# Performance work log

Measured on AMD Instinct MI355X. Metric: run time of the kernel, lower is better.

The kernel has to match this reference:

```python
import jax, jax.numpy as jnp
import numpy as np

L, D, H, FF = 24, 512, 16, 2048   # n_layer, hidden_dim, heads, mlp hidden
XLEN, YLEN = 1024, 1024
EPS = 1e-5


def setup_inputs() -> dict:
    key = jax.random.key(0)
    ks = jax.random.split(key, 6)
    S = XLEN + YLEN
    s = 0.02
    return {
        "x": jax.random.normal(ks[0], (1, S, D), jnp.float32),
        "qkv_w": jax.random.normal(ks[1], (L, 3 * D, D), jnp.float32) * s,
        "qkv_b": jnp.zeros((L, 3 * D), jnp.float32),
        "out_w": jax.random.normal(ks[2], (L, D, D), jnp.float32) * s,
        "out_b": jnp.zeros((L, D), jnp.float32),
        "w1": jax.random.normal(ks[3], (L, FF, D), jnp.float32) * s,
        "b1": jnp.zeros((L, FF), jnp.float32),
        "w2": jax.random.normal(ks[4], (L, D, FF), jnp.float32) * s,
        "b2": jnp.zeros((L, D), jnp.float32),
        "norm_w1": jnp.ones((L, D), jnp.float32),
        "norm_b1": jnp.zeros((L, D), jnp.float32),
        "norm_w2": jnp.ones((L, D), jnp.float32),
        "norm_b2": jnp.zeros((L, D), jnp.float32),
        "x_len": XLEN,
        "y_len": YLEN,
    }


def _layer_norm(h, w, b):
    m = h.mean(-1, keepdims=True)
    v = ((h - m) ** 2).mean(-1, keepdims=True)
    return (h - m) * jax.lax.rsqrt(v + EPS) * w + b


def _build_mask(x_len, y_len):
    # text rows: attend to all text, never to audio; audio rows: causal over audio, full over text
    top = jnp.concatenate([jnp.zeros((x_len, x_len), bool), jnp.ones((x_len, y_len), bool)], axis=1)
    bot = jnp.concatenate([jnp.zeros((y_len, x_len), bool), jnp.triu(jnp.ones((y_len, y_len), bool), 1)], axis=1)
    bm = jnp.concatenate([top, bot], axis=0)
    # canonical_mask: bool -> additive float with -100000 at masked positions
    return jnp.where(bm, jnp.float32(-100000.0), jnp.float32(0.0))


def reference(x, qkv_w, qkv_b, out_w, out_b, w1, b1, w2, b2, norm_w1, norm_b1, norm_w2, norm_b2, x_len, y_len):
    B, S, _ = x.shape
    hd = D // H
    scale = 1.0 / np.sqrt(hd)
    mask = _build_mask(x_len, y_len)  # [S, S]

    def layer(h, p):
        qw, qb, ow, ob, W1, B1, W2, B2, nw1, nb1, nw2, nb2 = p
        qkv = h @ qw.T + qb                                   # [B,S,3D]
        q, k, v = jnp.split(qkv, 3, axis=-1)
        q = q.reshape(B, S, H, hd).transpose(0, 2, 1, 3)      # [B,H,S,hd]
        k = k.reshape(B, S, H, hd).transpose(0, 2, 1, 3)
        v = v.reshape(B, S, H, hd).transpose(0, 2, 1, 3)
        att = jax.nn.softmax(jnp.einsum('bhqd,bhkd->bhqk', q, k) * scale + mask, axis=-1)
        o = jnp.einsum('bhqk,bhkd->bhqd', att, v).transpose(0, 2, 1, 3).reshape(B, S, D)
        o = o @ ow.T + ob
        h = _layer_norm(h + o, nw1, nb1)
        m = jax.nn.relu(h @ W1.T + B1) @ W2.T + B2            # T2SMLP
        h = _layer_norm(h + m, nw2, nb2)
        return h, None

    params = (qkv_w, qkv_b, out_w, out_b, w1, b1, w2, b2, norm_w1, norm_b1, norm_w2, norm_b2)
    x, _ = jax.lax.scan(layer, x, params)
    return x
```

## Files before the change

### kernel.cpp

```cpp
#include <hip/hip_runtime.h>
#include <cstddef>

#define S_LEN 2048
#define XLEN_C 1024
#define DMODEL 512
#define NHEAD 16
#define HDIM 32
#define FFDIM 2048
#define NLAYER 24
#define TD3 1536

typedef __attribute__((ext_vector_type(4))) float f32x4;
typedef __attribute__((ext_vector_type(8))) short short8;

__device__ __forceinline__ void split2(float x, unsigned short& h, unsigned short& l) {
  unsigned u = __float_as_uint(x);
  unsigned r = u + 0x7FFFu + ((u >> 16) & 1u);
  h = (unsigned short)(r >> 16);
  float hf = __uint_as_float((unsigned)h << 16);
  float lo = x - hf;
  unsigned u2 = __float_as_uint(lo);
  unsigned r2 = u2 + 0x7FFFu + ((u2 >> 16) & 1u);
  l = (unsigned short)(r2 >> 16);
}

template<int WMF, bool RELU, bool SPLIT_OUT>
__global__ __launch_bounds__(256) void gemm_mfma(const unsigned short* __restrict__ Ahg,
                                                 const unsigned short* __restrict__ Alg,
                                                 const float* __restrict__ Bg,
                                                 const float* __restrict__ bias,
                                                 float* __restrict__ Cf,
                                                 unsigned short* __restrict__ Ch,
                                                 unsigned short* __restrict__ Cl,
                                                 int N, int K) {
  constexpr int BM = 32 * WMF;
  __shared__ __align__(16) unsigned short Ahs[BM][40];
  __shared__ __align__(16) unsigned short Als[BM][40];
  __shared__ __align__(16) unsigned short Bhs[64][40];
  __shared__ __align__(16) unsigned short Bls[64][40];

  const int tid  = threadIdx.x;
  const int m0   = blockIdx.y * BM;
  const int n0   = blockIdx.x << 6;
  const int w    = tid >> 6;
  const int lane = tid & 63;
  const int wm   = (w >> 1) * (16 * WMF);
  const int wn   = (w & 1) << 5;
  const int fr   = lane & 15;
  const int fq   = lane >> 4;

  const int br = tid >> 2, bc = (tid & 3) << 3;

  f32x4 acc[WMF][2];
  #pragma unroll
  for (int i = 0; i < WMF; ++i)
    #pragma unroll
    for (int j = 0; j < 2; ++j)
      acc[i][j] = (f32x4){0.f, 0.f, 0.f, 0.f};

  for (int k0 = 0; k0 < K; k0 += 32) {
    float4 b0 = *(const float4*)&Bg[(size_t)(n0 + br) * K + k0 + bc];
    float4 b1 = *(const float4*)&Bg[(size_t)(n0 + br) * K + k0 + bc + 4];
    short8 bh, bl;
    {
      const float bf[8] = {b0.x, b0.y, b0.z, b0.w, b1.x, b1.y, b1.z, b1.w};
      #pragma unroll
      for (int i = 0; i < 8; ++i) {
        unsigned short h, lo; split2(bf[i], h, lo);
        bh[i] = (short)h; bl[i] = (short)lo;
      }
    }
    short8 a_h[(BM * 4) / 256], a_l[(BM * 4) / 256];
    #pragma unroll
    for (int it = 0; it < (BM * 4) / 256; ++it) {
      const int c = tid + (it << 8);
      const int arow = c >> 2, acol = (c & 3) << 3;
      a_h[it] = *(const short8*)&Ahg[(size_t)(m0 + arow) * K + k0 + acol];
      a_l[it] = *(const short8*)&Alg[(size_t)(m0 + arow) * K + k0 + acol];
    }
    __syncthreads();
    #pragma unroll
    for (int it = 0; it < (BM * 4) / 256; ++it) {
      const int c = tid + (it << 8);
      const int arow = c >> 2, acol = (c & 3) << 3;
      *(short8*)&Ahs[arow][acol] = a_h[it];
      *(short8*)&Als[arow][acol] = a_l[it];
    }
    *(short8*)&Bhs[br][bc] = bh;
    *(short8*)&Bls[br][bc] = bl;
    __syncthreads();

    short8 fah[WMF], fal[WMF], fbh[2], fbl[2];
    #pragma unroll
    for (int fm = 0; fm < WMF; ++fm) {
      fah[fm] = *(const short8*)&Ahs[wm + (fm << 4) + fr][fq << 3];
      fal[fm] = *(const short8*)&Als[wm + (fm << 4) + fr][fq << 3];
    }
    #pragma unroll
    for (int fn = 0; fn < 2; ++fn) {
      fbh[fn] = *(const short8*)&Bhs[wn + (fn << 4) + fr][fq << 3];
      fbl[fn] = *(const short8*)&Bls[wn + (fn << 4) + fr][fq << 3];
    }
    #pragma unroll
    for (int fm = 0; fm < WMF; ++fm)
      #pragma unroll
      for (int fn = 0; fn < 2; ++fn) {
        acc[fm][fn] = __builtin_amdgcn_mfma_f32_16x16x32_bf16(fah[fm], fbh[fn], acc[fm][fn], 0, 0, 0);
        acc[fm][fn] = __builtin_amdgcn_mfma_f32_16x16x32_bf16(fah[fm], fbl[fn], acc[fm][fn], 0, 0, 0);
        acc[fm][fn] = __builtin_amdgcn_mfma_f32_16x16x32_bf16(fal[fm], fbh[fn], acc[fm][fn], 0, 0, 0);
      }
  }

  #pragma unroll
  for (int fn = 0; fn < 2; ++fn) {
    const int col = n0 + wn + (fn << 4) + fr;
    const float bb = bias[col];
    #pragma unroll
    for (int fm = 0; fm < WMF; ++fm) {
      const int rbase = m0 + wm + (fm << 4) + (fq << 2);
      #pragma unroll
      for (int i = 0; i < 4; ++i) {
        float v = acc[fm][fn][i] + bb;
        if (RELU) v = fmaxf(v, 0.f);
        const size_t idx = (size_t)(rbase + i) * N + col;
        if (SPLIT_OUT) {
          unsigned short h, lo; split2(v, h, lo);
          Ch[idx] = h; Cl[idx] = lo;
        } else {
          Cf[idx] = v;
        }
      }
    }
  }
}

__global__ __launch_bounds__(256) void attn_mfma(const unsigned short* __restrict__ qh_g,
                                                 const unsigned short* __restrict__ ql_g,
                                                 unsigned short* __restrict__ oh_g,
                                                 unsigned short* __restrict__ ol_g) {
  const int hh  = blockIdx.x;
  const int q0  = blockIdx.y << 6;
  const int tid = threadIdx.x;
  const int w   = tid >> 6;
  const int lane = tid & 63;
  const int fr = lane & 15;
  const int fq = lane >> 4;
  constexpr float SCALE = 0.17677669529663687f;

  __shared__ __align__(16) unsigned short Kh[64][40];
  __shared__ __align__(16) unsigned short Kl[64][40];
  __shared__ __align__(16) unsigned short Vth[32][72];
  __shared__ __align__(16) unsigned short Vtl[32][72];
  __shared__ __align__(16) unsigned short Ph[4][16][72];
  __shared__ __align__(16) unsigned short Pl[4][16][72];

  const int qrow = q0 + (w << 4) + fr;
  const short8 fQh = *(const short8*)&qh_g[(size_t)qrow * TD3 + hh * HDIM + (fq << 3)];
  const short8 fQl = *(const short8*)&ql_g[(size_t)qrow * TD3 + hh * HDIM + (fq << 3)];

  float m = -3.0e38f, l = 0.f;
  f32x4 accO[2];
  accO[0] = (f32x4){0.f, 0.f, 0.f, 0.f};
  accO[1] = (f32x4){0.f, 0.f, 0.f, 0.f};

  const int kend   = (q0 < XLEN_C) ? XLEN_C : (q0 + 64);
  const int ntiles = kend >> 6;

  const int krow = tid >> 2, kcol = (tid & 3) << 3;
  const int vd = tid & 31, vseg = tid >> 5;

  for (int t = 0; t < ntiles; ++t) {
    const int c0 = t << 6;
    __syncthreads();
    *(short8*)&Kh[krow][kcol] =
        *(const short8*)&qh_g[(size_t)(c0 + krow) * TD3 + DMODEL + hh * HDIM + kcol];
    *(short8*)&Kl[krow][kcol] =
        *(const short8*)&ql_g[(size_t)(c0 + krow) * TD3 + DMODEL + hh * HDIM + kcol];
    short8 vh8, vl8;
    #pragma unroll
    for (int j = 0; j < 8; ++j) {
      const size_t ga = (size_t)(c0 + (vseg << 3) + j) * TD3 + 2 * DMODEL + hh * HDIM + vd;
      vh8[j] = (short)qh_g[ga];
      vl8[j] = (short)ql_g[ga];
    }
    *(short8*)&Vth[vd][vseg << 3] = vh8;
    *(short8*)&Vtl[vd][vseg << 3] = vl8;
    __syncthreads();

    f32x4 s4[4];
    #pragma unroll
    for (int sub = 0; sub < 4; ++sub) {
      s4[sub] = (f32x4){0.f, 0.f, 0.f, 0.f};
      const short8 kh = *(const short8*)&Kh[(sub << 4) + fr][fq << 3];
      const short8 kl = *(const short8*)&Kl[(sub << 4) + fr][fq << 3];
      s4[sub] = __builtin_amdgcn_mfma_f32_16x16x32_bf16(kh, fQh, s4[sub], 0, 0, 0);
      s4[sub] = __builtin_amdgcn_mfma_f32_16x16x32_bf16(kh, fQl, s4[sub], 0, 0, 0);
      s4[sub] = __builtin_amdgcn_mfma_f32_16x16x32_bf16(kl, fQh, s4[sub], 0, 0, 0);
    }

    float sv[16];
    float tmax = -3.0e38f;
    #pragma unroll
    for (int sub = 0; sub < 4; ++sub)
      #pragma unroll
      for (int i = 0; i < 4; ++i) {
        const int k = c0 + (sub << 4) + (fq << 2) + i;
        const bool ok = (k < XLEN_C) | (k <= qrow);
        const float val = ok ? s4[sub][i] * SCALE : -3.0e38f;
        sv[(sub << 2) + i] = val;
        tmax = fmaxf(tmax, val);
      }
    tmax = fmaxf(tmax, __shfl_xor(tmax, 16));
    tmax = fmaxf(tmax, __shfl_xor(tmax, 32));
    const float mnew  = fmaxf(m, tmax);
    const float alpha = __expf(m - mnew);
    m = mnew;
    float psum = 0.f;
    unsigned short p_h[16], p_l[16];
    #pragma unroll
    for (int idx = 0; idx < 16; ++idx) {
      const float p = __expf(sv[idx] - mnew);
      psum += p;
      split2(p, p_h[idx], p_l[idx]);
    }
    psum += __shfl_xor(psum, 16);
    psum += __shfl_xor(psum, 32);
    l = l * alpha + psum;

    #pragma unroll
    for (int sub = 0; sub < 4; ++sub) {
      ushort4 uh, ul;
      uh.x = p_h[(sub << 2) + 0]; uh.y = p_h[(sub << 2) + 1];
      uh.z = p_h[(sub << 2) + 2]; uh.w = p_h[(sub << 2) + 3];
      ul.x = p_l[(sub << 2) + 0]; ul.y = p_l[(sub << 2) + 1];
      ul.z = p_l[(sub << 2) + 2]; ul.w = p_l[(sub << 2) + 3];
      *(ushort4*)&Ph[w][fr][(sub << 4) + (fq << 2)] = uh;
      *(ushort4*)&Pl[w][fr][(sub << 4) + (fq << 2)] = ul;
    }

    const float a0 = __shfl(alpha, (fq << 2) + 0);
    const float a1 = __shfl(alpha, (fq << 2) + 1);
    const float a2 = __shfl(alpha, (fq << 2) + 2);
    const float a3 = __shfl(alpha, (fq << 2) + 3);
    #pragma unroll
    for (int df = 0; df < 2; ++df) {
      accO[df][0] *= a0; accO[df][1] *= a1;
      accO[df][2] *= a2; accO[df][3] *= a3;
    }

    #pragma unroll
    for (int kh2 = 0; kh2 < 2; ++kh2) {
      const short8 pah = *(const short8*)&Ph[w][fr][(kh2 << 5) + (fq << 3)];
      const short8 pal = *(const short8*)&Pl[w][fr][(kh2 << 5) + (fq << 3)];
      #pragma unroll
      for (int df = 0; df < 2; ++df) {
        const short8 vbh = *(const short8*)&Vth[(df << 4) + fr][(kh2 << 5) + (fq << 3)];
        const short8 vbl = *(const short8*)&Vtl[(df << 4) + fr][(kh2 << 5) + (fq << 3)];
        accO[df] = __builtin_amdgcn_mfma_f32_16x16x32_bf16(pah, vbh, accO[df], 0, 0, 0);
        accO[df] = __builtin_amdgcn_mfma_f32_16x16x32_bf16(pal, vbh, accO[df], 0, 0, 0);
        accO[df] = __builtin_amdgcn_mfma_f32_16x16x32_bf16(pah, vbl, accO[df], 0, 0, 0);
      }
    }
  }

  const float linv = 1.f / l;
  const float l0 = __shfl(linv, (fq << 2) + 0);
  const float l1 = __shfl(linv, (fq << 2) + 1);
  const float l2v = __shfl(linv, (fq << 2) + 2);
  const float l3 = __shfl(linv, (fq << 2) + 3);
  #pragma unroll
  for (int df = 0; df < 2; ++df) {
    const int col = hh * HDIM + (df << 4) + fr;
    const float vals[4] = {accO[df][0] * l0, accO[df][1] * l1,
                           accO[df][2] * l2v, accO[df][3] * l3};
    #pragma unroll
    for (int i = 0; i < 4; ++i) {
      const int row = q0 + (w << 4) + (fq << 2) + i;
      unsigned short h, lo; split2(vals[i], h, lo);
      oh_g[(size_t)row * DMODEL + col] = h;
      ol_g[(size_t)row * DMODEL + col] = lo;
    }
  }
}

__global__ __launch_bounds__(256) void add_layernorm(const float* __restrict__ h,
                                                     const float* __restrict__ r,
                                                     const float* __restrict__ w,
                                                     const float* __restrict__ b,
                                                     float* __restrict__ out,
                                                     unsigned short* __restrict__ oh,
                                                     unsigned short* __restrict__ ol) {
  const int row = blockIdx.x;
  const int tid = threadIdx.x;
  const float2 hv = *(const float2*)&h[(size_t)row * DMODEL + tid * 2];
  const float2 rv = *(const float2*)&r[(size_t)row * DMODEL + tid * 2];
  const float a0 = hv.x + rv.x, a1 = hv.y + rv.y;
  float s = a0 + a1, ss = a0 * a0 + a1 * a1;
  #pragma unroll
  for (int off = 32; off; off >>= 1) {
    s  += __shfl_xor(s, off);
    ss += __shfl_xor(ss, off);
  }
  __shared__ float sb[4], ssb[4];
  const int wid = tid >> 6;
  if ((tid & 63) == 0) { sb[wid] = s; ssb[wid] = ss; }
  __syncthreads();
  s  = sb[0] + sb[1] + sb[2] + sb[3];
  ss = ssb[0] + ssb[1] + ssb[2] + ssb[3];
  const float mean = s * (1.f / DMODEL);
  const float var  = ss * (1.f / DMODEL) - mean * mean;
  const float rs   = rsqrtf(var + 1e-5f);
  const float2 wv = *(const float2*)&w[tid * 2];
  const float2 bv = *(const float2*)&b[tid * 2];
  const float o0 = (a0 - mean) * rs * wv.x + bv.x;
  const float o1 = (a1 - mean) * rs * wv.y + bv.y;
  float2 o; o.x = o0; o.y = o1;
  *(float2*)&out[(size_t)row * DMODEL + tid * 2] = o;
  unsigned short h0, l0, h1, l1;
  split2(o0, h0, l0); split2(o1, h1, l1);
  ushort2 uh; uh.x = h0; uh.y = h1;
  ushort2 ul; ul.x = l0; ul.y = l1;
  *(ushort2*)&oh[(size_t)row * DMODEL + tid * 2] = uh;
  *(ushort2*)&ol[(size_t)row * DMODEL + tid * 2] = ul;
}

__global__ __launch_bounds__(256) void split_init(const float* __restrict__ x,
                                                  float* __restrict__ f,
                                                  unsigned short* __restrict__ h,
                                                  unsigned short* __restrict__ l,
                                                  int n4) {
  const int i = blockIdx.x * 256 + threadIdx.x;
  if (i >= n4) return;
  const float4 v = *(const float4*)&x[i * 4];
  *(float4*)&f[i * 4] = v;
  const float vf[4] = {v.x, v.y, v.z, v.w};
  ushort4 uh, ul;
  unsigned short hh, ll;
  split2(vf[0], hh, ll); uh.x = hh; ul.x = ll;
  split2(vf[1], hh, ll); uh.y = hh; ul.y = ll;
  split2(vf[2], hh, ll); uh.z = hh; ul.z = ll;
  split2(vf[3], hh, ll); uh.w = hh; ul.w = ll;
  *(ushort4*)&h[i * 4] = uh;
  *(ushort4*)&l[i * 4] = ul;
}

extern "C" void kernel_launch(void* const* d_in, const int* in_sizes, int n_in,
                              void* d_out, int out_size, void* d_ws, size_t ws_size,
                              hipStream_t stream) {
  const float* x     = (const float*)d_in[0];
  const float* qkv_w = (const float*)d_in[1];
  const float* qkv_b = (const float*)d_in[2];
  const float* out_w = (const float*)d_in[3];
  const float* out_b = (const float*)d_in[4];
  const float* w1    = (const float*)d_in[5];
  const float* b1    = (const float*)d_in[6];
  const float* w2    = (const float*)d_in[7];
  const float* b2    = (const float*)d_in[8];
  const float* nw1   = (const float*)d_in[9];
  const float* nb1   = (const float*)d_in[10];
  const float* nw2   = (const float*)d_in[11];
  const float* nb2   = (const float*)d_in[12];

  char* p = (char*)d_ws;
  float* Hc = (float*)p;              p += (size_t)S_LEN * DMODEL * 4;
  unsigned short* Hh = (unsigned short*)p;   p += (size_t)S_LEN * DMODEL * 2;
  unsigned short* Hl = (unsigned short*)p;   p += (size_t)S_LEN * DMODEL * 2;
  unsigned short* qkvh = (unsigned short*)p; p += (size_t)S_LEN * TD3 * 2;
  unsigned short* qkvl = (unsigned short*)p; p += (size_t)S_LEN * TD3 * 2;
  unsigned short* oath = (unsigned short*)p; p += (size_t)S_LEN * DMODEL * 2;
  unsigned short* oatl = (unsigned short*)p; p += (size_t)S_LEN * DMODEL * 2;
  float* opr = (float*)p;             p += (size_t)S_LEN * DMODEL * 4;
  unsigned short* midh = (unsigned short*)p; p += (size_t)S_LEN * FFDIM * 2;
  unsigned short* midl = (unsigned short*)p; p += (size_t)S_LEN * FFDIM * 2;

  split_init<<<(S_LEN * DMODEL / 4 + 255) / 256, 256, 0, stream>>>(
      x, Hc, Hh, Hl, S_LEN * DMODEL / 4);

  for (int l = 0; l < NLAYER; ++l) {
    const float* qw = qkv_w + (size_t)l * TD3 * DMODEL;
    const float* qb = qkv_b + (size_t)l * TD3;
    const float* ow = out_w + (size_t)l * DMODEL * DMODEL;
    const float* ob = out_b + (size_t)l * DMODEL;
    const float* W1 = w1 + (size_t)l * FFDIM * DMODEL;
    const float* B1 = b1 + (size_t)l * FFDIM;
    const float* W2 = w2 + (size_t)l * DMODEL * FFDIM;
    const float* B2 = b2 + (size_t)l * DMODEL;

    gemm_mfma<4, false, true><<<dim3(TD3 / 64, S_LEN / 128), 256, 0, stream>>>(
        Hh, Hl, qw, qb, nullptr, qkvh, qkvl, TD3, DMODEL);
    attn_mfma<<<dim3(NHEAD, S_LEN / 64), 256, 0, stream>>>(qkvh, qkvl, oath, oatl);
    gemm_mfma<2, false, false><<<dim3(DMODEL / 64, S_LEN / 64), 256, 0, stream>>>(
        oath, oatl, ow, ob, opr, nullptr, nullptr, DMODEL, DMODEL);
    add_layernorm<<<S_LEN, 256, 0, stream>>>(
        Hc, opr, nw1 + (size_t)l * DMODEL, nb1 + (size_t)l * DMODEL, Hc, Hh, Hl);
    gemm_mfma<4, true, true><<<dim3(FFDIM / 64, S_LEN / 128), 256, 0, stream>>>(
        Hh, Hl, W1, B1, nullptr, midh, midl, FFDIM, DMODEL);
    gemm_mfma<2, false, false><<<dim3(DMODEL / 64, S_LEN / 64), 256, 0, stream>>>(
        midh, midl, W2, B2, opr, nullptr, nullptr, DMODEL, FFDIM);
    add_layernorm<<<S_LEN, 256, 0, stream>>>(
        Hc, opr, nw2 + (size_t)l * DMODEL, nb2 + (size_t)l * DMODEL, Hc, Hh, Hl);
  }

  hipMemcpyAsync(d_out, Hc, sizeof(float) * S_LEN * DMODEL,
                 hipMemcpyDeviceToDevice, stream);
}
```

Baseline: 5.827 ms.

## Pre-split weights to bf16 hi/lo, pre-transpose V, use exp2 softmax

The weights are converted once per call into bf16 high/low pairs, so the GEMM kernels load pre-split halves instead of re-splitting fp32 weights in every tile. A separate transpose kernel writes V in head-major transposed layout, so attention loads V with vector reads instead of strided scalar gathers. The softmax scale is folded with log2(e) so it can use exp2f. The cost is a large extra workspace (weights are only pre-split if it fits), extra split kernels at startup, and one more launch per layer.

Result: faster. 5.287 ms (-9.3%).

```diff
diff --git a/kernel.cpp b/kernel.cpp
--- a/kernel.cpp
+++ b/kernel.cpp
@@ -24,10 +24,12 @@
   l = (unsigned short)(r2 >> 16);
 }
 
-template<int WMF, bool RELU, bool SPLIT_OUT>
+template<int WMF, bool RELU, bool SPLIT_OUT, bool PRESPLIT_B>
 __global__ __launch_bounds__(256) void gemm_mfma(const unsigned short* __restrict__ Ahg,
                                                  const unsigned short* __restrict__ Alg,
                                                  const float* __restrict__ Bg,
+                                                 const unsigned short* __restrict__ Bhg,
+                                                 const unsigned short* __restrict__ Blg,
                                                  const float* __restrict__ bias,
                                                  float* __restrict__ Cf,
                                                  unsigned short* __restrict__ Ch,
@@ -59,10 +61,13 @@
       acc[i][j] = (f32x4){0.f, 0.f, 0.f, 0.f};
 
   for (int k0 = 0; k0 < K; k0 += 32) {
-    float4 b0 = *(const float4*)&Bg[(size_t)(n0 + br) * K + k0 + bc];
-    float4 b1 = *(const float4*)&Bg[(size_t)(n0 + br) * K + k0 + bc + 4];
     short8 bh, bl;
-    {
+    if (PRESPLIT_B) {
+      bh = *(const short8*)&Bhg[(size_t)(n0 + br) * K + k0 + bc];
+      bl = *(const short8*)&Blg[(size_t)(n0 + br) * K + k0 + bc];
+    } else {
+      float4 b0 = *(const float4*)&Bg[(size_t)(n0 + br) * K + k0 + bc];
+      float4 b1 = *(const float4*)&Bg[(size_t)(n0 + br) * K + k0 + bc + 4];
       const float bf[8] = {b0.x, b0.y, b0.z, b0.w, b1.x, b1.y, b1.z, b1.w};
       #pragma unroll
       for (int i = 0; i < 8; ++i) {
@@ -134,8 +139,33 @@
   }
 }
 
+__global__ __launch_bounds__(256) void transpose_v(const unsigned short* __restrict__ qh,
+                                                   const unsigned short* __restrict__ ql,
+                                                   unsigned short* __restrict__ vth,
+                                                   unsigned short* __restrict__ vtl) {
+  const int hh  = blockIdx.x;
+  const int t0  = blockIdx.y << 6;
+  const int tid = threadIdx.x;
+  __shared__ unsigned short Th[64][40];
+  __shared__ unsigned short Tl[64][40];
+  const int lseq = tid >> 2, dg = (tid & 3) << 3;
+  const size_t src = (size_t)(t0 + lseq) * TD3 + 2 * DMODEL + (hh << 5) + dg;
+  *(short8*)&Th[lseq][dg] = *(const short8*)&qh[src];
+  *(short8*)&Tl[lseq][dg] = *(const short8*)&ql[src];
+  __syncthreads();
+  const int d = tid >> 3, sg = (tid & 7) << 3;
+  short8 oh, ol;
+  #pragma unroll
+  for (int j = 0; j < 8; ++j) { oh[j] = (short)Th[sg + j][d]; ol[j] = (short)Tl[sg + j][d]; }
+  const size_t dst = ((size_t)(hh << 5) + d) * S_LEN + t0 + sg;
+  *(short8*)&vth[dst] = oh;
+  *(short8*)&vtl[dst] = ol;
+}
+
 __global__ __launch_bounds__(256) void attn_mfma(const unsigned short* __restrict__ qh_g,
                                                  const unsigned short* __restrict__ ql_g,
+                                                 const unsigned short* __restrict__ vth_g,
+                                                 const unsigned short* __restrict__ vtl_g,
                                                  unsigned short* __restrict__ oh_g,
                                                  unsigned short* __restrict__ ol_g) {
   const int hh  = blockIdx.x;
@@ -145,7 +175,7 @@
   const int lane = tid & 63;
   const int fr = lane & 15;
   const int fq = lane >> 4;
-  constexpr float SCALE = 0.17677669529663687f;
+  constexpr float SCL2 = 0.17677669529663687f * 1.44269504088896341f;
 
   __shared__ __align__(16) unsigned short Kh[64][40];
   __shared__ __align__(16) unsigned short Kl[64][40];
@@ -167,7 +197,7 @@
   const int ntiles = kend >> 6;
 
   const int krow = tid >> 2, kcol = (tid & 3) << 3;
-  const int vd = tid & 31, vseg = tid >> 5;
+  const int vd = tid >> 3, vseg = tid & 7;
 
   for (int t = 0; t < ntiles; ++t) {
     const int c0 = t << 6;
@@ -176,15 +206,9 @@
         *(const short8*)&qh_g[(size_t)(c0 + krow) * TD3 + DMODEL + hh * HDIM + kcol];
     *(short8*)&Kl[krow][kcol] =
         *(const short8*)&ql_g[(size_t)(c0 + krow) * TD3 + DMODEL + hh * HDIM + kcol];
-    short8 vh8, vl8;
-    #pragma unroll
-    for (int j = 0; j < 8; ++j) {
-      const size_t ga = (size_t)(c0 + (vseg << 3) + j) * TD3 + 2 * DMODEL + hh * HDIM + vd;
-      vh8[j] = (short)qh_g[ga];
-      vl8[j] = (short)ql_g[ga];
-    }
-    *(short8*)&Vth[vd][vseg << 3] = vh8;
-    *(short8*)&Vtl[vd][vseg << 3] = vl8;
+    const size_t vsrc = ((size_t)(hh << 5) + vd) * S_LEN + c0 + (vseg << 3);
+    *(short8*)&Vth[vd][vseg << 3] = *(const short8*)&vth_g[vsrc];
+    *(short8*)&Vtl[vd][vseg << 3] = *(const short8*)&vtl_g[vsrc];
     __syncthreads();
 
     f32x4 s4[4];
@@ -206,20 +230,20 @@
       for (int i = 0; i < 4; ++i) {
         const int k = c0 + (sub << 4) + (fq << 2) + i;
         const bool ok = (k < XLEN_C) | (k <= qrow);
-        const float val = ok ? s4[sub][i] * SCALE : -3.0e38f;
+        const float val = ok ? s4[sub][i] * SCL2 : -3.0e38f;
         sv[(sub << 2) + i] = val;
         tmax = fmaxf(tmax, val);
       }
     tmax = fmaxf(tmax, __shfl_xor(tmax, 16));
     tmax = fmaxf(tmax, __shfl_xor(tmax, 32));
     const float mnew  = fmaxf(m, tmax);
-    const float alpha = __expf(m - mnew);
+    const float alpha = exp2f(m - mnew);
     m = mnew;
     float psum = 0.f;
     unsigned short p_h[16], p_l[16];
     #pragma unroll
     for (int idx = 0; idx < 16; ++idx) {
-      const float p = __expf(sv[idx] - mnew);
+      const float p = exp2f(sv[idx] - mnew);
       psum += p;
       split2(p, p_h[idx], p_l[idx]);
     }
@@ -324,6 +348,22 @@
   *(ushort2*)&ol[(size_t)row * DMODEL + tid * 2] = ul;
 }
 
+__global__ __launch_bounds__(256) void split_w(const float* __restrict__ src,
+                                               unsigned short* __restrict__ h,
+                                               unsigned short* __restrict__ l) {
+  const int i = blockIdx.x * 256 + threadIdx.x;
+  const float4 v = *(const float4*)&src[(size_t)i * 4];
+  const float vf[4] = {v.x, v.y, v.z, v.w};
+  ushort4 uh, ul;
+  unsigned short hh, ll;
+  split2(vf[0], hh, ll); uh.x = hh; ul.x = ll;
+  split2(vf[1], hh, ll); uh.y = hh; ul.y = ll;
+  split2(vf[2], hh, ll); uh.z = hh; ul.z = ll;
+  split2(vf[3], hh, ll); uh.w = hh; ul.w = ll;
+  *(ushort4*)&h[(size_t)i * 4] = uh;
+  *(ushort4*)&l[(size_t)i * 4] = ul;
+}
+
 __global__ __launch_bounds__(256) void split_init(const float* __restrict__ x,
                                                   float* __restrict__ f,
                                                   unsigned short* __restrict__ h,
@@ -331,8 +371,8 @@
                                                   int n4) {
   const int i = blockIdx.x * 256 + threadIdx.x;
   if (i >= n4) return;
-  const float4 v = *(const float4*)&x[i * 4];
-  *(float4*)&f[i * 4] = v;
+  const float4 v = *(const float4*)&x[(size_t)i * 4];
+  *(float4*)&f[(size_t)i * 4] = v;
   const float vf[4] = {v.x, v.y, v.z, v.w};
   ushort4 uh, ul;
   unsigned short hh, ll;
@@ -340,8 +380,8 @@
   split2(vf[1], hh, ll); uh.y = hh; ul.y = ll;
   split2(vf[2], hh, ll); uh.z = hh; ul.z = ll;
   split2(vf[3], hh, ll); uh.w = hh; ul.w = ll;
-  *(ushort4*)&h[i * 4] = uh;
-  *(ushort4*)&l[i * 4] = ul;
+  *(ushort4*)&h[(size_t)i * 4] = uh;
+  *(ushort4*)&l[(size_t)i * 4] = ul;
 }
 
 extern "C" void kernel_launch(void* const* d_in, const int* in_sizes, int n_in,
@@ -362,19 +402,38 @@
   const float* nb2   = (const float*)d_in[12];
 
   char* p = (char*)d_ws;
-  float* Hc = (float*)p;              p += (size_t)S_LEN * DMODEL * 4;
+  float* Hc = (float*)p;                     p += (size_t)S_LEN * DMODEL * 4;
   unsigned short* Hh = (unsigned short*)p;   p += (size_t)S_LEN * DMODEL * 2;
   unsigned short* Hl = (unsigned short*)p;   p += (size_t)S_LEN * DMODEL * 2;
   unsigned short* qkvh = (unsigned short*)p; p += (size_t)S_LEN * TD3 * 2;
   unsigned short* qkvl = (unsigned short*)p; p += (size_t)S_LEN * TD3 * 2;
   unsigned short* oath = (unsigned short*)p; p += (size_t)S_LEN * DMODEL * 2;
   unsigned short* oatl = (unsigned short*)p; p += (size_t)S_LEN * DMODEL * 2;
-  float* opr = (float*)p;             p += (size_t)S_LEN * DMODEL * 4;
+  float* opr = (float*)p;                    p += (size_t)S_LEN * DMODEL * 4;
   unsigned short* midh = (unsigned short*)p; p += (size_t)S_LEN * FFDIM * 2;
   unsigned short* midl = (unsigned short*)p; p += (size_t)S_LEN * FFDIM * 2;
+  unsigned short* vth = (unsigned short*)p;  p += (size_t)S_LEN * DMODEL * 2;
+  unsigned short* vtl = (unsigned short*)p;  p += (size_t)S_LEN * DMODEL * 2;
+  unsigned short* qkvWh = (unsigned short*)p; p += (size_t)NLAYER * TD3 * DMODEL * 2;
+  unsigned short* qkvWl = (unsigned short*)p; p += (size_t)NLAYER * TD3 * DMODEL * 2;
+  unsigned short* outWh = (unsigned short*)p; p += (size_t)NLAYER * DMODEL * DMODEL * 2;
+  unsigned short* outWl = (unsigned short*)p; p += (size_t)NLAYER * DMODEL * DMODEL * 2;
+  unsigned short* w1h = (unsigned short*)p;   p += (size_t)NLAYER * FFDIM * DMODEL * 2;
+  unsigned short* w1l = (unsigned short*)p;   p += (size_t)NLAYER * FFDIM * DMODEL * 2;
+  unsigned short* w2h = (unsigned short*)p;   p += (size_t)NLAYER * DMODEL * FFDIM * 2;
+  unsigned short* w2l = (unsigned short*)p;   p += (size_t)NLAYER * DMODEL * FFDIM * 2;
+  const size_t need = (size_t)(p - (char*)d_ws);
+  const bool presplit = ws_size >= need;
 
   split_init<<<(S_LEN * DMODEL / 4 + 255) / 256, 256, 0, stream>>>(
       x, Hc, Hh, Hl, S_LEN * DMODEL / 4);
+
+  if (presplit) {
+    split_w<<<NLAYER * TD3 * DMODEL / 1024, 256, 0, stream>>>(qkv_w, qkvWh, qkvWl);
+    split_w<<<NLAYER * DMODEL * DMODEL / 1024, 256, 0, stream>>>(out_w, outWh, outWl);
+    split_w<<<NLAYER * FFDIM * DMODEL / 1024, 256, 0, stream>>>(w1, w1h, w1l);
+    split_w<<<NLAYER * DMODEL * FFDIM / 1024, 256, 0, stream>>>(w2, w2h, w2l);
+  }
 
   for (int l = 0; l < NLAYER; ++l) {
     const float* qw = qkv_w + (size_t)l * TD3 * DMODEL;
@@ -386,19 +445,46 @@
     const float* W2 = w2 + (size_t)l * DMODEL * FFDIM;
     const float* B2 = b2 + (size_t)l * DMODEL;
 
-    gemm_mfma<4, false, true><<<dim3(TD3 / 64, S_LEN / 128), 256, 0, stream>>>(
-        Hh, Hl, qw, qb, nullptr, qkvh, qkvl, TD3, DMODEL);
-    attn_mfma<<<dim3(NHEAD, S_LEN / 64), 256, 0, stream>>>(qkvh, qkvl, oath, oatl);
-    gemm_mfma<2, false, false><<<dim3(DMODEL / 64, S_LEN / 64), 256, 0, stream>>>(
-        oath, oatl, ow, ob, opr, nullptr, nullptr, DMODEL, DMODEL);
-    add_layernorm<<<S_LEN, 256, 0, stream>>>(
-        Hc, opr, nw1 + (size_t)l * DMODEL, nb1 + (size_t)l * DMODEL, Hc, Hh, Hl);
-    gemm_mfma<4, true, true><<<dim3(FFDIM / 64, S_LEN / 128), 256, 0, stream>>>(
-        Hh, Hl, W1, B1, nullptr, midh, midl, FFDIM, DMODEL);
-    gemm_mfma<2, false, false><<<dim3(DMODEL / 64, S_LEN / 64), 256, 0, stream>>>(
-        midh, midl, W2, B2, opr, nullptr, nullptr, DMODEL, FFDIM);
-    add_layernorm<<<S_LEN, 256, 0, stream>>>(
-        Hc, opr, nw2 + (size_t)l * DMODEL, nb2 + (size_t)l * DMODEL, Hc, Hh, Hl);
+    if (presplit) {
+      const unsigned short* qwh = qkvWh + (size_t)l * TD3 * DMODEL;
+      const unsigned short* qwl = qkvWl + (size_t)l * TD3 * DMODEL;
+      const unsigned short* owh = outWh + (size_t)l * DMODEL * DMODEL;
+      const unsigned short* owl = outWl + (size_t)l * DMODEL * DMODEL;
+      const unsigned short* W1h = w1h + (size_t)l * FFDIM * DMODEL;
+      const unsigned short* W1l = w1l + (size_t)l * FFDIM * DMODEL;
+      const unsigned short* W2h = w2h + (size_t)l * DMODEL * FFDIM;
+      const unsigned short* W2l = w2l + (size_t)l * DMODEL * FFDIM;
+
+      gemm_mfma<4, false, true, true><<<dim3(TD3 / 64, S_LEN / 128), 256, 0, stream>>>(
+          Hh, Hl, nullptr, qwh, qwl, qb, nullptr, qkvh, qkvl, TD3, DMODEL);
+      transpose_v<<<dim3(NHEAD, S_LEN / 64), 256, 0, stream>>>(qkvh, qkvl, vth, vtl);
+      attn_mfma<<<dim3(NHEAD, S_LEN / 64), 256, 0, stream>>>(qkvh, qkvl, vth, vtl, oath, oatl);
+      gemm_mfma<2, false, false, true><<<dim3(DMODEL / 64, S_LEN / 64), 256, 0, stream>>>(
+          oath, oatl, nullptr, owh, owl, ob, opr, nullptr, nullptr, DMODEL, DMODEL);
+      add_layernorm<<<S_LEN, 256, 0, stream>>>(
+          Hc, opr, nw1 + (size_t)l * DMODEL, nb1 + (size_t)l * DMODEL, Hc, Hh, Hl);
+      gemm_mfma<4, true, true, true><<<dim3(FFDIM / 64, S_LEN / 128), 256, 0, stream>>>(
+          Hh, Hl, nullptr, W1h, W1l, B1, nullptr, midh, midl, FFDIM, DMODEL);
+      gemm_mfma<2, false, false, true><<<dim3(DMODEL / 64, S_LEN / 64), 256, 0, stream>>>(
+          midh, midl, nullptr, W2h, W2l, B2, opr, nullptr, nullptr, DMODEL, FFDIM);
+      add_layernorm<<<S_LEN, 256, 0, stream>>>(
+          Hc, opr, nw2 + (size_t)l * DMODEL, nb2 + (size_t)l * DMODEL, Hc, Hh, Hl);
+    } else {
+      gemm_mfma<4, false, true, false><<<dim3(TD3 / 64, S_LEN / 128), 256, 0, stream>>>(
+          Hh, Hl, qw, nullptr, nullptr, qb, nullptr, qkvh, qkvl, TD3, DMODEL);
+      transpose_v<<<dim3(NHEAD, S_LEN / 64), 256, 0, stream>>>(qkvh, qkvl, vth, vtl);
+      attn_mfma<<<dim3(NHEAD, S_LEN / 64), 256, 0, stream>>>(qkvh, qkvl, vth, vtl, oath, oatl);
+      gemm_mfma<2, false, false, false><<<dim3(DMODEL / 64, S_LEN / 64), 256, 0, stream>>>(
+          oath, oatl, ow, nullptr, nullptr, ob, opr, nullptr, nullptr, DMODEL, DMODEL);
+      add_layernorm<<<S_LEN, 256, 0, stream>>>(
+          Hc, opr, nw1 + (size_t)l * DMODEL, nb1 + (size_t)l * DMODEL, Hc, Hh, Hl);
+      gemm_mfma<4, true, true, false><<<dim3(FFDIM / 64, S_LEN / 128), 256, 0, stream>>>(
+          Hh, Hl, W1, nullptr, nullptr, B1, nullptr, midh, midl, FFDIM, DMODEL);
+      gemm_mfma<2, false, false, false><<<dim3(DMODEL / 64, S_LEN / 64), 256, 0, stream>>>(
+          midh, midl, W2, nullptr, nullptr, B2, opr, nullptr, nullptr, DMODEL, FFDIM);
+      add_layernorm<<<S_LEN, 256, 0, stream>>>(
+          Hc, opr, nw2 + (size_t)l * DMODEL, nb2 + (size_t)l * DMODEL, Hc, Hh, Hl);
+    }
   }
 
   hipMemcpyAsync(d_out, Hc, sizeof(float) * S_LEN * DMODEL,
```
